# Kernel optimization log

Measured on AMD Instinct MI355X. Metric: run time of the kernel, lower is better.

Reference implementation:

```python
import jax, jax.numpy as jnp
import numpy as np

HEADS = 16
DIM_HEAD = 64
SCALE = DIM_HEAD ** -0.5


def setup_inputs() -> dict:
    key = jax.random.key(0)
    k1, k2, k3 = jax.random.split(key, 3)
    B, N, D = 8, 1024, 1024
    x = jax.random.normal(k1, (B, N, D), dtype=jnp.float32)
    # 0/1 keep-mask over the N-1 non-prepended positions
    mask = jax.random.randint(k2, (B, N - 1), 0, 2, dtype=jnp.int32)
    # Linear(dim, 3*inner_dim, bias=False); stored as [dim, 3*inner] so y = x @ W
    w_qkv = jax.random.normal(k3, (D, 3 * HEADS * DIM_HEAD), dtype=jnp.float32) * (D ** -0.5)
    return {"x": x, "mask": mask, "w_qkv": w_qkv}


def reference(x, mask, w_qkv):
    b, n, _ = x.shape
    h, d = HEADS, DIM_HEAD
    qkv = x @ w_qkv                                    # [b, n, 3*h*d]
    q, k, v = jnp.split(qkv, 3, axis=-1)
    to_heads = lambda t: t.reshape(b, n, h, d).transpose(0, 2, 1, 3)  # b h n d
    q, k, v = to_heads(q), to_heads(k), to_heads(v)
    dots = jnp.einsum('bhid,bhjd->bhij', q, k) * SCALE  # [b, h, n, n]
    # F.pad(mask.flatten(1), (1,0), value=1.0) -> prepend a kept position
    m = jnp.pad(mask.reshape(b, -1).astype(jnp.float32), ((0, 0), (1, 0)),
                constant_values=1.0)                    # [b, n]
    dots = dots - 10000.0 * (1.0 - m)[:, None, None, :]
    attn = jax.nn.softmax(dots, axis=-1)
    out = jnp.einsum('bhij,bhjd->bhid', attn, v)        # [b, h, n, d]
    return out.transpose(0, 2, 1, 3).reshape(b, n, h * d)
```

## Files before the change

### kernel.cpp

```cpp
#include <hip/hip_runtime.h>
#include <hip/hip_bf16.h>
#include <stdint.h>

#define HEADS 16
#define DH    64
#define SEQ   1024
#define DIM   1024

typedef __attribute__((ext_vector_type(8))) short bf16x8;
typedef __attribute__((ext_vector_type(4))) float f32x4;
typedef __attribute__((ext_vector_type(16))) float f32x16;
typedef __attribute__((ext_vector_type(4))) unsigned int u32x4;

#define QSCALE_L2 0.18033688011112042f
#define THR_L2 11.541560327111707f
#define PEN_L2 (-14427.0f)

static __device__ __forceinline__ unsigned short f2bf(float f) {
  unsigned u = __builtin_bit_cast(unsigned, f);
  u += 0x7fff + ((u >> 16) & 1);
  return (unsigned short)(u >> 16);
}

static __device__ __forceinline__ float fexp2(float x) {
#if __has_builtin(__builtin_amdgcn_exp2f)
  return __builtin_amdgcn_exp2f(x);
#else
  return exp2f(x);
#endif
}

static __device__ __forceinline__ void gload_lds16(const void* g, void* l) {
  __builtin_amdgcn_global_load_lds(
      (const __attribute__((address_space(1))) unsigned int*)g,
      (__attribute__((address_space(3))) unsigned int*)l,
      16, 0, 0);
}

__global__ __launch_bounds__(256) void build_keep(
    const int* __restrict__ mask, int* __restrict__ inv, int* __restrict__ nkeep) {
  const int b = blockIdx.x;
  const int t = threadIdx.x;
  __shared__ int sc[256];
  int kept[4];
  int c = 0;
#pragma unroll
  for (int k = 0; k < 4; ++k) {
    const int j = t * 4 + k;
    const int kp = (j == 0) ? 1 : (mask[b * (SEQ - 1) + j - 1] != 0);
    kept[k] = kp;
    c += kp;
  }
  sc[t] = c;
  __syncthreads();
  for (int off = 1; off < 256; off <<= 1) {
    const int v = (t >= off) ? sc[t - off] : 0;
    __syncthreads();
    sc[t] += v;
    __syncthreads();
  }
  int pos = sc[t] - c;
  const int total = sc[255];
#pragma unroll
  for (int k = 0; k < 4; ++k) {
    const int j = t * 4 + k;
    inv[b * SEQ + j] = kept[k] ? pos : -1;
    pos += kept[k];
  }
  if (t == 0) nkeep[b] = total;
}

__global__ __launch_bounds__(256) void cvt_x(
    const float* __restrict__ in, unsigned short* __restrict__ out) {
  const int i = (blockIdx.x * 256 + threadIdx.x) * 4;
  const float4 v = *reinterpret_cast<const float4*>(in + i);
  short4 o;
  o.x = (short)f2bf(v.x);
  o.y = (short)f2bf(v.y);
  o.z = (short)f2bf(v.z);
  o.w = (short)f2bf(v.w);
  *reinterpret_cast<short4*>(out + i) = o;
}

__global__ __launch_bounds__(256) void transpose_w(
    const float* __restrict__ w, unsigned short* __restrict__ wT) {
  __shared__ unsigned short t[64][68];
  const int tid = threadIdx.x;
  const int bk = blockIdx.x;
  const int bn = blockIdx.y;
  const int r = tid >> 4;
  const int c = (tid & 15) * 4;
#pragma unroll
  for (int rr = 0; rr < 64; rr += 16) {
    const float4 v = *reinterpret_cast<const float4*>(
        w + (size_t)(bk * 64 + r + rr) * 3072 + bn * 64 + c);
    t[r + rr][c + 0] = f2bf(v.x);
    t[r + rr][c + 1] = f2bf(v.y);
    t[r + rr][c + 2] = f2bf(v.z);
    t[r + rr][c + 3] = f2bf(v.w);
  }
  __syncthreads();
#pragma unroll
  for (int rr = 0; rr < 64; rr += 16) {
    short4 o;
    o.x = (short)t[c + 0][r + rr];
    o.y = (short)t[c + 1][r + rr];
    o.z = (short)t[c + 2][r + rr];
    o.w = (short)t[c + 3][r + rr];
    *reinterpret_cast<short4*>(
        wT + (size_t)(bn * 64 + r + rr) * 1024 + bk * 64 + c) = o;
  }
}

__global__ __launch_bounds__(256) void qkv_gemm(
    const unsigned short* __restrict__ x, const unsigned short* __restrict__ wT,
    const int* __restrict__ inv,
    unsigned short* __restrict__ Qh, unsigned short* __restrict__ Kc,
    unsigned short* __restrict__ Vc) {
  __shared__ alignas(16) unsigned char L[2][2][16384];
  const int tid = threadIdx.x;
  const int lane = tid & 63;
  const int wave = tid >> 6;
  const int m0 = blockIdx.x * 128;
  const int n0 = blockIdx.y * 128;
  const int wm = (wave >> 1) * 64;
  const int wn = (wave & 1) * 64;
  const int l15 = lane & 15;
  const int lg = lane >> 4;
  const int lg4 = lg * 4;

  f32x4 acc[4][4] = {};

  auto STAGE = [&](int buf, int kt) {
#pragma unroll
    for (int r = 0; r < 4; ++r) {
      const int o = r * 4096 + tid * 16;
      const int row = o >> 7;
      const int sch = ((o >> 4) & 7) ^ (row & 7);
      gload_lds16(x + (size_t)(m0 + row) * DIM + kt + sch * 8, &L[buf][0][o]);
      gload_lds16(wT + (size_t)(n0 + row) * DIM + kt + sch * 8, &L[buf][1][o]);
    }
  };

  STAGE(0, 0);

  for (int t = 0; t < 16; ++t) {
    const int kt = t * 64;
    if (t < 15) {
      STAGE((t + 1) & 1, kt + 64);
      asm volatile("s_waitcnt vmcnt(8)" ::: "memory");
    } else {
      asm volatile("s_waitcnt vmcnt(0)" ::: "memory");
    }
    __builtin_amdgcn_s_barrier();

    const unsigned char* Abuf = &L[t & 1][0][0];
    const unsigned char* Bbuf = &L[t & 1][1][0];
    bf16x8 af[4][2], bfr[4][2];
#pragma unroll
    for (int i = 0; i < 4; ++i) {
#pragma unroll
      for (int kk = 0; kk < 2; ++kk) {
        const int ra = wm + i * 16 + l15;
        af[i][kk] = *reinterpret_cast<const bf16x8*>(
            Abuf + ra * 128 + (((kk * 4 + lg) ^ (ra & 7)) << 4));
        const int rb = wn + i * 16 + l15;
        bfr[i][kk] = *reinterpret_cast<const bf16x8*>(
            Bbuf + rb * 128 + (((kk * 4 + lg) ^ (rb & 7)) << 4));
      }
    }
#pragma unroll
    for (int kk = 0; kk < 2; ++kk)
#pragma unroll
      for (int i = 0; i < 4; ++i)
#pragma unroll
        for (int j = 0; j < 4; ++j)
          acc[i][j] = __builtin_amdgcn_mfma_f32_16x16x32_bf16(
              af[i][kk], bfr[j][kk], acc[i][j], 0, 0, 0);

    __builtin_amdgcn_s_barrier();
  }

  unsigned short* Sw = reinterpret_cast<unsigned short*>(&L[0][0][0] + wave * 2304);
  const int sec = n0 >> 10;
  const float sc = (sec == 0) ? QSCALE_L2 : 1.0f;
  const int h = ((n0 + wn) >> 6) & 15;
#pragma unroll
  for (int i = 0; i < 4; ++i) {
#pragma unroll
    for (int j = 0; j < 4; ++j)
#pragma unroll
      for (int r = 0; r < 4; ++r)
        Sw[(lg4 + r) * 72 + j * 16 + l15] = f2bf(acc[i][j][r] * sc);
#pragma unroll
    for (int pass = 0; pass < 2; ++pass) {
      const int row = pass * 8 + (lane >> 3);
      const int chunk = lane & 7;
      const bf16x8 vv = *reinterpret_cast<const bf16x8*>(&Sw[row * 72 + chunk * 8]);
      const int grow = m0 + wm + i * 16 + row;
      const int b = grow >> 10;
      const int n = grow & 1023;
      const size_t bh = (size_t)b * HEADS + h;
      if (sec == 0) {
        *reinterpret_cast<bf16x8*>(&Qh[(bh * SEQ + n) * DH + chunk * 8]) = vv;
      } else {
        const int iv = inv[b * SEQ + n];
        if (iv >= 0) {
          if (sec == 1)
            *reinterpret_cast<bf16x8*>(&Kc[(bh * SEQ + iv) * DH + chunk * 8]) = vv;
          else
            *reinterpret_cast<bf16x8*>(&Vc[(bh * SEQ + iv) * DH + chunk * 8]) = vv;
        }
      }
    }
  }
}

__global__ __launch_bounds__(256) void transpose_v(
    const unsigned short* __restrict__ Vc, unsigned short* __restrict__ Vtc) {
  __shared__ unsigned short t[64][72];
  const int tid = threadIdx.x;
  const int i0 = blockIdx.x * 64;
  const int bhi = blockIdx.y;
  const unsigned short* src = Vc + (size_t)bhi * SEQ * DH;
  unsigned short* dst = Vtc + (size_t)bhi * DH * SEQ;
  const int r = tid >> 3;
  const int c = (tid & 7) * 8;
#pragma unroll
  for (int rr = 0; rr < 64; rr += 32) {
    const bf16x8 v = *reinterpret_cast<const bf16x8*>(
        src + (size_t)(i0 + r + rr) * DH + c);
    *reinterpret_cast<bf16x8*>(&t[r + rr][c]) = v;
  }
  __syncthreads();
#pragma unroll
  for (int dd = 0; dd < 64; dd += 32) {
    const int d = r + dd;
    bf16x8 o;
#pragma unroll
    for (int e = 0; e < 8; ++e) o[e] = (short)t[c + e][d];
    *reinterpret_cast<bf16x8*>(dst + (size_t)d * SEQ + i0 + c) = o;
  }
}

__global__ __launch_bounds__(256) void attn_fwd5(
    const unsigned short* __restrict__ Qh, const unsigned short* __restrict__ Kc,
    const unsigned short* __restrict__ Vtc,
    const int* __restrict__ nkeep, float* __restrict__ out) {
  __shared__ alignas(16) unsigned char Kl[2][8192];
  __shared__ alignas(16) unsigned char Vl[2][8192];
  __shared__ float corrw[4][32];
  const int tid = threadIdx.x;
  const int lane = tid & 63;
  const int wave = tid >> 6;
  const int l31 = lane & 31;
  const int hi = lane >> 5;
  const int h8 = hi * 8;
  const bool islo = lane < 32;

  const int bid = ((blockIdx.x & 7) << 7) | (blockIdx.x >> 3);
  const int b = bid >> 7;
  const int hh = (bid >> 3) & 15;
  const int qc = bid & 7;
  const size_t bh = (size_t)b * HEADS + hh;
  const int q0 = qc * 128 + wave * 32;

  const int nk = nkeep[b];
  const int ntile = (nk + 63) >> 6;

  const unsigned short* Q = Qh + bh * SEQ * DH;
  const unsigned short* K = Kc + bh * SEQ * DH;
  const unsigned short* V = Vtc + bh * DH * SEQ;

  auto STAGE = [&](int buf, int kt) {
#pragma unroll
    for (int p = 0; p < 2; ++p) {
      const int off = p * 4096 + tid * 16;
      const int row = off >> 7;
      const int chunk = (off >> 4) & 7;
      const int sch = chunk ^ (row & 7);
      gload_lds16(K + (size_t)(kt + row) * DH + sch * 8, &Kl[buf][off]);
      gload_lds16(V + (size_t)row * SEQ + kt + sch * 8, &Vl[buf][off]);
    }
  };

  STAGE(0, 0);

  bf16x8 qf[4];
#pragma unroll
  for (int ds = 0; ds < 4; ++ds)
    qf[ds] = *reinterpret_cast<const bf16x8*>(
        Q + (size_t)(q0 + l31) * DH + ds * 16 + h8);

  u32x4 onesu = {0u, 0u, 0u, 0u};
  onesu.x = islo ? 0x3F80u : 0u;
  const bf16x8 onesf = __builtin_bit_cast(bf16x8, onesu);

  f32x16 Od0 = (f32x16)0.f, Od1 = (f32x16)0.f;
  float m_ = 0.f, l_ = 0.f;

  __syncthreads();

  int cur = 0;
  for (int ti = 0; ti < ntile; ++ti) {
    const int kt = ti * 64;
    if (ti + 1 < ntile) STAGE(cur ^ 1, kt + 64);

    f32x16 st0 = (f32x16)0.f, st1 = (f32x16)0.f;
    __builtin_amdgcn_s_setprio(1);
#pragma unroll
    for (int ds = 0; ds < 4; ++ds) {
      const int c0 = (ds * 2 + hi) ^ (l31 & 7);
      const bf16x8 kf0 = *reinterpret_cast<const bf16x8*>(
          &Kl[cur][l31 * 128 + c0 * 16]);
      st0 = __builtin_amdgcn_mfma_f32_32x32x16_bf16(kf0, qf[ds], st0, 0, 0, 0);
      const bf16x8 kf1 = *reinterpret_cast<const bf16x8*>(
          &Kl[cur][(32 + l31) * 128 + c0 * 16]);
      st1 = __builtin_amdgcn_mfma_f32_32x32x16_bf16(kf1, qf[ds], st1, 0, 0, 0);
    }
    __builtin_amdgcn_s_setprio(0);

    if (ti == ntile - 1) {
      const unsigned short pv = f2bf(PEN_L2);
      const unsigned short pu0 = (kt + l31 < nk) ? (unsigned short)0 : pv;
      const unsigned short pu1 = (kt + 32 + l31 < nk) ? (unsigned short)0 : pv;
      u32x4 p0 = {0u, 0u, 0u, 0u}, p1 = {0u, 0u, 0u, 0u};
      p0.x = islo ? (unsigned)pu0 : 0u;
      p1.x = islo ? (unsigned)pu1 : 0u;
      st0 = __builtin_amdgcn_mfma_f32_32x32x16_bf16(
          __builtin_bit_cast(bf16x8, p0), onesf, st0, 0, 0, 0);
      st1 = __builtin_amdgcn_mfma_f32_32x32x16_bf16(
          __builtin_bit_cast(bf16x8, p1), onesf, st1, 0, 0, 0);
    }
    float a[8];
#pragma unroll
    for (int i = 0; i < 8; ++i)
      a[i] = fmaxf(fmaxf(st0[i], st0[i + 8]), fmaxf(st1[i], st1[i + 8]));
#pragma unroll
    for (int k = 4; k >= 1; k >>= 1)
#pragma unroll
      for (int i = 0; i < k; ++i) a[i] = fmaxf(a[i], a[i + k]);
    const float mx = fmaxf(a[0], __shfl_xor(a[0], 32));
    if (!__all(mx <= m_ + THR_L2)) {
      const float mn = fmaxf(m_, mx);
      const float corr = fexp2(m_ - mn);
      m_ = mn;
      l_ *= corr;
      if (islo) corrw[wave][l31] = corr;
      f32x4 cv[4];
#pragma unroll
      for (int j = 0; j < 4; ++j)
        cv[j] = *reinterpret_cast<const f32x4*>(&corrw[wave][j * 8 + (h8 >> 1)]);
#pragma unroll
      for (int r = 0; r < 16; ++r) {
        Od0[r] *= cv[r >> 2][r & 3];
        Od1[r] *= cv[r >> 2][r & 3];
      }
    }
#pragma unroll
    for (int i = 0; i < 16; ++i) {
      st0[i] = fexp2(st0[i] - m_);
      st1[i] = fexp2(st1[i] - m_);
    }
    float s8[8];
#pragma unroll
    for (int i = 0; i < 8; ++i)
      s8[i] = (st0[i] + st0[i + 8]) + (st1[i] + st1[i + 8]);
#pragma unroll
    for (int k = 4; k >= 1; k >>= 1)
#pragma unroll
      for (int i = 0; i < k; ++i) s8[i] += s8[i + k];
    l_ += s8[0] + __shfl_xor(s8[0], 32);
    bf16x8 pf[4];
#pragma unroll
    for (int t = 0; t < 2; ++t) {
#pragma unroll
      for (int bq = 0; bq < 2; ++bq) {
        const int o = 8 * bq;
        float e0 = t ? st1[o + 0] : st0[o + 0], e1 = t ? st1[o + 1] : st0[o + 1];
        float e2 = t ? st1[o + 2] : st0[o + 2], e3 = t ? st1[o + 3] : st0[o + 3];
        float e4 = t ? st1[o + 4] : st0[o + 4], e5 = t ? st1[o + 5] : st0[o + 5];
        float e6 = t ? st1[o + 6] : st0[o + 6], e7 = t ? st1[o + 7] : st0[o + 7];
        unsigned A0, A1, B0, B1;
        asm("v_cvt_pk_bf16_f32 %0, %1, %2" : "=v"(A0) : "v"(e0), "v"(e1));
        asm("v_cvt_pk_bf16_f32 %0, %1, %2" : "=v"(A1) : "v"(e2), "v"(e3));
        asm("v_cvt_pk_bf16_f32 %0, %1, %2" : "=v"(B0) : "v"(e4), "v"(e5));
        asm("v_cvt_pk_bf16_f32 %0, %1, %2" : "=v"(B1) : "v"(e6), "v"(e7));
        asm("v_permlane32_swap_b32 %0, %1\n\ts_nop 1" : "+v"(A0), "+v"(B0));
        asm("v_permlane32_swap_b32 %0, %1\n\ts_nop 1" : "+v"(A1), "+v"(B1));
        u32x4 pk4;
        pk4.x = A0; pk4.y = A1; pk4.z = B0; pk4.w = B1;
        pf[t * 2 + bq] = __builtin_bit_cast(bf16x8, pk4);
      }
    }
    __builtin_amdgcn_s_setprio(1);
#pragma unroll
    for (int kvs = 0; kvs < 4; ++kvs) {
      const int c0 = (kvs * 2 + hi) ^ (l31 & 7);
      const bf16x8 v0 = *reinterpret_cast<const bf16x8*>(
          &Vl[cur][l31 * 128 + c0 * 16]);
      Od0 = __builtin_amdgcn_mfma_f32_32x32x16_bf16(pf[kvs], v0, Od0, 0, 0, 0);
      const bf16x8 v1 = *reinterpret_cast<const bf16x8*>(
          &Vl[cur][(32 + l31) * 128 + c0 * 16]);
      Od1 = __builtin_amdgcn_mfma_f32_32x32x16_bf16(pf[kvs], v1, Od1, 0, 0, 0);
    }
    __builtin_amdgcn_s_setprio(0);

    __syncthreads();
    cur ^= 1;
  }

  if (islo) corrw[wave][l31] = 1.0f / l_;
  f32x4 lv[4];
#pragma unroll
  for (int j = 0; j < 4; ++j)
    lv[j] = *reinterpret_cast<const f32x4*>(&corrw[wave][j * 8 + (h8 >> 1)]);
#pragma unroll
  for (int r = 0; r < 16; ++r) {
    const int q = q0 + (r & 3) + 8 * (r >> 2) + (hi << 2);
    out[((size_t)b * SEQ + q) * (HEADS * DH) + hh * DH + 0 * 32 + l31] =
        Od0[r] * lv[r >> 2][r & 3];
    out[((size_t)b * SEQ + q) * (HEADS * DH) + hh * DH + 1 * 32 + l31] =
        Od1[r] * lv[r >> 2][r & 3];
  }
}

extern "C" void kernel_launch(void* const* d_in, const int* in_sizes, int n_in,
                              void* d_out, int out_size, void* d_ws, size_t ws_size,
                              hipStream_t stream) {
  const float* x = (const float*)d_in[0];
  const int* mask = (const int*)d_in[1];
  const float* w = (const float*)d_in[2];
  float* outp = (float*)d_out;

  char* ws = (char*)d_ws;
  unsigned short* xb   = (unsigned short*)(ws);
  unsigned short* wT   = (unsigned short*)(ws + 16777216);
  unsigned short* Qh   = (unsigned short*)(ws + 23068672);
  unsigned short* Kc   = (unsigned short*)(ws + 39845888);
  unsigned short* Vc   = (unsigned short*)(ws + 56623104);
  int*            inv  = (int*)(ws + 73400320);
  int*            nkp  = (int*)(ws + 73433088);
  unsigned short* Vtc  = xb;

  build_keep<<<dim3(8), 256, 0, stream>>>(mask, inv, nkp);
  cvt_x<<<dim3(8192), 256, 0, stream>>>(x, xb);
  transpose_w<<<dim3(16, 48), 256, 0, stream>>>(w, wT);
  qkv_gemm<<<dim3(64, 24), 256, 0, stream>>>(xb, wT, inv, Qh, Kc, Vc);
  transpose_v<<<dim3(16, 128), 256, 0, stream>>>(Vc, Vtc);
  attn_fwd5<<<dim3(1024), 256, 0, stream>>>(Qh, Kc, Vtc, nkp, outp);
}
```

Measured before the change: 134.8 us.

## Merge prep kernels and enlarge QKV GEMM tile to 256x128 single-buffered

Measured after the change: 125.7 us. 1.07x faster.

```diff
diff --git a/kernel.cpp b/kernel.cpp
--- a/kernel.cpp
+++ b/kernel.cpp
@@ -37,156 +37,155 @@
       16, 0, 0);
 }
 
-__global__ __launch_bounds__(256) void build_keep(
-    const int* __restrict__ mask, int* __restrict__ inv, int* __restrict__ nkeep) {
-  const int b = blockIdx.x;
-  const int t = threadIdx.x;
+__global__ __launch_bounds__(256) void prep(
+    const float* __restrict__ x, unsigned short* __restrict__ xb,
+    const float* __restrict__ w, unsigned short* __restrict__ wT,
+    const int* __restrict__ mask, int* __restrict__ inv,
+    int* __restrict__ nkeep) {
+  __shared__ unsigned short t[64][68];
   __shared__ int sc[256];
-  int kept[4];
-  int c = 0;
-#pragma unroll
-  for (int k = 0; k < 4; ++k) {
-    const int j = t * 4 + k;
-    const int kp = (j == 0) ? 1 : (mask[b * (SEQ - 1) + j - 1] != 0);
-    kept[k] = kp;
-    c += kp;
-  }
-  sc[t] = c;
-  __syncthreads();
-  for (int off = 1; off < 256; off <<= 1) {
-    const int v = (t >= off) ? sc[t - off] : 0;
+  const int bidx = blockIdx.x;
+  const int tid = threadIdx.x;
+
+  if (bidx < 8192) {
+    const int i = (bidx * 256 + tid) * 4;
+    const float4 v = *reinterpret_cast<const float4*>(x + i);
+    short4 o;
+    o.x = (short)f2bf(v.x);
+    o.y = (short)f2bf(v.y);
+    o.z = (short)f2bf(v.z);
+    o.w = (short)f2bf(v.w);
+    *reinterpret_cast<short4*>(xb + i) = o;
+  } else if (bidx < 8960) {
+    const int lin = bidx - 8192;
+    const int bk = lin & 15;
+    const int bn = lin >> 4;
+    const int r = tid >> 4;
+    const int c = (tid & 15) * 4;
+#pragma unroll
+    for (int rr = 0; rr < 64; rr += 16) {
+      const float4 v = *reinterpret_cast<const float4*>(
+          w + (size_t)(bk * 64 + r + rr) * 3072 + bn * 64 + c);
+      t[r + rr][c + 0] = f2bf(v.x);
+      t[r + rr][c + 1] = f2bf(v.y);
+      t[r + rr][c + 2] = f2bf(v.z);
+      t[r + rr][c + 3] = f2bf(v.w);
+    }
     __syncthreads();
-    sc[t] += v;
+#pragma unroll
+    for (int rr = 0; rr < 64; rr += 16) {
+      short4 o;
+      o.x = (short)t[c + 0][r + rr];
+      o.y = (short)t[c + 1][r + rr];
+      o.z = (short)t[c + 2][r + rr];
+      o.w = (short)t[c + 3][r + rr];
+      *reinterpret_cast<short4*>(
+          wT + (size_t)(bn * 64 + r + rr) * 1024 + bk * 64 + c) = o;
+    }
+  } else {
+    const int b = bidx - 8960;
+    int kept[4];
+    int c = 0;
+#pragma unroll
+    for (int k = 0; k < 4; ++k) {
+      const int j = tid * 4 + k;
+      const int kp = (j == 0) ? 1 : (mask[b * (SEQ - 1) + j - 1] != 0);
+      kept[k] = kp;
+      c += kp;
+    }
+    sc[tid] = c;
     __syncthreads();
-  }
-  int pos = sc[t] - c;
-  const int total = sc[255];
-#pragma unroll
-  for (int k = 0; k < 4; ++k) {
-    const int j = t * 4 + k;
-    inv[b * SEQ + j] = kept[k] ? pos : -1;
-    pos += kept[k];
-  }
-  if (t == 0) nkeep[b] = total;
-}
-
-__global__ __launch_bounds__(256) void cvt_x(
-    const float* __restrict__ in, unsigned short* __restrict__ out) {
-  const int i = (blockIdx.x * 256 + threadIdx.x) * 4;
-  const float4 v = *reinterpret_cast<const float4*>(in + i);
-  short4 o;
-  o.x = (short)f2bf(v.x);
-  o.y = (short)f2bf(v.y);
-  o.z = (short)f2bf(v.z);
-  o.w = (short)f2bf(v.w);
-  *reinterpret_cast<short4*>(out + i) = o;
-}
-
-__global__ __launch_bounds__(256) void transpose_w(
-    const float* __restrict__ w, unsigned short* __restrict__ wT) {
-  __shared__ unsigned short t[64][68];
-  const int tid = threadIdx.x;
-  const int bk = blockIdx.x;
-  const int bn = blockIdx.y;
-  const int r = tid >> 4;
-  const int c = (tid & 15) * 4;
-#pragma unroll
-  for (int rr = 0; rr < 64; rr += 16) {
-    const float4 v = *reinterpret_cast<const float4*>(
-        w + (size_t)(bk * 64 + r + rr) * 3072 + bn * 64 + c);
-    t[r + rr][c + 0] = f2bf(v.x);
-    t[r + rr][c + 1] = f2bf(v.y);
-    t[r + rr][c + 2] = f2bf(v.z);
-    t[r + rr][c + 3] = f2bf(v.w);
-  }
-  __syncthreads();
-#pragma unroll
-  for (int rr = 0; rr < 64; rr += 16) {
-    short4 o;
-    o.x = (short)t[c + 0][r + rr];
-    o.y = (short)t[c + 1][r + rr];
-    o.z = (short)t[c + 2][r + rr];
-    o.w = (short)t[c + 3][r + rr];
-    *reinterpret_cast<short4*>(
-        wT + (size_t)(bn * 64 + r + rr) * 1024 + bk * 64 + c) = o;
-  }
-}
-
-__global__ __launch_bounds__(256) void qkv_gemm(
+    for (int off = 1; off < 256; off <<= 1) {
+      const int v = (tid >= off) ? sc[tid - off] : 0;
+      __syncthreads();
+      sc[tid] += v;
+      __syncthreads();
+    }
+    int pos = sc[tid] - c;
+    const int total = sc[255];
+#pragma unroll
+    for (int k = 0; k < 4; ++k) {
+      const int j = tid * 4 + k;
+      inv[b * SEQ + j] = kept[k] ? pos : -1;
+      pos += kept[k];
+    }
+    if (tid == 0) nkeep[b] = total;
+  }
+}
+
+__global__ __launch_bounds__(256, 2) void qkv_gemm(
     const unsigned short* __restrict__ x, const unsigned short* __restrict__ wT,
     const int* __restrict__ inv,
     unsigned short* __restrict__ Qh, unsigned short* __restrict__ Kc,
     unsigned short* __restrict__ Vc) {
-  __shared__ alignas(16) unsigned char L[2][2][16384];
+  __shared__ alignas(16) unsigned char La[256 * 128];
+  __shared__ alignas(16) unsigned char Lb[128 * 128];
   const int tid = threadIdx.x;
   const int lane = tid & 63;
   const int wave = tid >> 6;
-  const int m0 = blockIdx.x * 128;
+  const int m0 = blockIdx.x * 256;
   const int n0 = blockIdx.y * 128;
-  const int wm = (wave >> 1) * 64;
+  const int wm = (wave >> 1) * 128;
   const int wn = (wave & 1) * 64;
   const int l15 = lane & 15;
   const int lg = lane >> 4;
   const int lg4 = lg * 4;
 
-  f32x4 acc[4][4] = {};
-
-  auto STAGE = [&](int buf, int kt) {
+  f32x4 acc[8][4] = {};
+
+  auto STAGE = [&](int kt) {
+#pragma unroll
+    for (int r = 0; r < 8; ++r) {
+      const int o = r * 4096 + tid * 16;
+      const int row = o >> 7;
+      const int sch = ((o >> 4) & 7) ^ (row & 7);
+      gload_lds16(x + (size_t)(m0 + row) * DIM + kt + sch * 8, La + o);
+    }
 #pragma unroll
     for (int r = 0; r < 4; ++r) {
       const int o = r * 4096 + tid * 16;
       const int row = o >> 7;
       const int sch = ((o >> 4) & 7) ^ (row & 7);
-      gload_lds16(x + (size_t)(m0 + row) * DIM + kt + sch * 8, &L[buf][0][o]);
-      gload_lds16(wT + (size_t)(n0 + row) * DIM + kt + sch * 8, &L[buf][1][o]);
+      gload_lds16(wT + (size_t)(n0 + row) * DIM + kt + sch * 8, Lb + o);
     }
   };
-
-  STAGE(0, 0);
 
   for (int t = 0; t < 16; ++t) {
     const int kt = t * 64;
-    if (t < 15) {
-      STAGE((t + 1) & 1, kt + 64);
-      asm volatile("s_waitcnt vmcnt(8)" ::: "memory");
-    } else {
-      asm volatile("s_waitcnt vmcnt(0)" ::: "memory");
-    }
-    __builtin_amdgcn_s_barrier();
-
-    const unsigned char* Abuf = &L[t & 1][0][0];
-    const unsigned char* Bbuf = &L[t & 1][1][0];
-    bf16x8 af[4][2], bfr[4][2];
-#pragma unroll
-    for (int i = 0; i < 4; ++i) {
-#pragma unroll
-      for (int kk = 0; kk < 2; ++kk) {
+    __syncthreads();
+    STAGE(kt);
+    __syncthreads();
+#pragma unroll
+    for (int kk = 0; kk < 2; ++kk) {
+      bf16x8 af[8], bfr[4];
+#pragma unroll
+      for (int i = 0; i < 8; ++i) {
         const int ra = wm + i * 16 + l15;
-        af[i][kk] = *reinterpret_cast<const bf16x8*>(
-            Abuf + ra * 128 + (((kk * 4 + lg) ^ (ra & 7)) << 4));
-        const int rb = wn + i * 16 + l15;
-        bfr[i][kk] = *reinterpret_cast<const bf16x8*>(
-            Bbuf + rb * 128 + (((kk * 4 + lg) ^ (rb & 7)) << 4));
+        af[i] = *reinterpret_cast<const bf16x8*>(
+            La + ra * 128 + (((kk * 4 + lg) ^ (ra & 7)) << 4));
       }
-    }
-#pragma unroll
-    for (int kk = 0; kk < 2; ++kk)
-#pragma unroll
-      for (int i = 0; i < 4; ++i)
+#pragma unroll
+      for (int j = 0; j < 4; ++j) {
+        const int rb = wn + j * 16 + l15;
+        bfr[j] = *reinterpret_cast<const bf16x8*>(
+            Lb + rb * 128 + (((kk * 4 + lg) ^ (rb & 7)) << 4));
+      }
+#pragma unroll
+      for (int i = 0; i < 8; ++i)
 #pragma unroll
         for (int j = 0; j < 4; ++j)
           acc[i][j] = __builtin_amdgcn_mfma_f32_16x16x32_bf16(
-              af[i][kk], bfr[j][kk], acc[i][j], 0, 0, 0);
-
-    __builtin_amdgcn_s_barrier();
-  }
-
-  unsigned short* Sw = reinterpret_cast<unsigned short*>(&L[0][0][0] + wave * 2304);
+              af[i], bfr[j], acc[i][j], 0, 0, 0);
+    }
+  }
+
+  __syncthreads();
+  unsigned short* Sw = reinterpret_cast<unsigned short*>(La + wave * 2304);
   const int sec = n0 >> 10;
   const float sc = (sec == 0) ? QSCALE_L2 : 1.0f;
   const int h = ((n0 + wn) >> 6) & 15;
 #pragma unroll
-  for (int i = 0; i < 4; ++i) {
+  for (int i = 0; i < 8; ++i) {
 #pragma unroll
     for (int j = 0; j < 4; ++j)
 #pragma unroll
@@ -443,10 +442,8 @@
   int*            nkp  = (int*)(ws + 73433088);
   unsigned short* Vtc  = xb;
 
-  build_keep<<<dim3(8), 256, 0, stream>>>(mask, inv, nkp);
-  cvt_x<<<dim3(8192), 256, 0, stream>>>(x, xb);
-  transpose_w<<<dim3(16, 48), 256, 0, stream>>>(w, wT);
-  qkv_gemm<<<dim3(64, 24), 256, 0, stream>>>(xb, wT, inv, Qh, Kc, Vc);
+  prep<<<dim3(8968), 256, 0, stream>>>(x, xb, w, wT, mask, inv, nkp);
+  qkv_gemm<<<dim3(32, 24), 256, 0, stream>>>(xb, wT, inv, Qh, Kc, Vc);
   transpose_v<<<dim3(16, 128), 256, 0, stream>>>(Vc, Vtc);
   attn_fwd5<<<dim3(1024), 256, 0, stream>>>(Qh, Kc, Vtc, nkp, outp);
 }
```
